# Optimization experiments

Measured on AMD Instinct MI355X. Metric: run time of the kernel, lower is better.

Reference implementation:

```python
import jax, jax.numpy as jnp
import numpy as np

N = 12288
D = 128
NUM_BATCH = 32
EPS = 1e-8


def setup_inputs() -> dict:
    key = jax.random.key(0)
    kq, kk, kv, kb = jax.random.split(key, 4)
    Q = jax.random.normal(kq, (N, D), dtype=jnp.float32)
    K = jax.random.normal(kk, (N, D), dtype=jnp.float32)
    V = jax.random.normal(kv, (N, D), dtype=jnp.float32)
    batch_seg = jnp.sort(jax.random.randint(kb, (N,), 0, NUM_BATCH, dtype=jnp.int32))
    return {"Q": Q, "K": K, "V": V, "num_batch": NUM_BATCH, "batch_seg": batch_seg}


def reference(Q, K, V, num_batch, batch_seg):
    d = Q.shape[-1]
    dot = Q @ K.T                                   # [N, N]
    # NOTE: faithful to original: subtract GLOBAL max, then divide by sqrt(d)
    A = jnp.exp((dot - jnp.max(dot)) / jnp.sqrt(jnp.float32(d)))
    if num_batch > 1:
        mask = (batch_seg[None, :] == batch_seg[:, None])  # block-diagonal
        A = jnp.where(mask, A, jnp.zeros((), A.dtype))
    norm = jnp.sum(A, axis=-1, keepdims=True) + EPS
    A_weights = A / norm
    return A_weights @ V
```

## Files before the change

### kernel.cpp

```cpp
#include <hip/hip_runtime.h>


#define NN 12288
#define DD 128
#define NB 32
#define PS_LD 40
#define VTS 12424

typedef __attribute__((ext_vector_type(8))) short short8;
typedef __attribute__((ext_vector_type(4))) float float4v;

__device__ __forceinline__ short f2bf(float f) {
  unsigned u = __builtin_bit_cast(unsigned, f);
  return (short)((u + 0x7FFFu + ((u >> 16) & 1u)) >> 16);
}

__device__ __forceinline__ short8 ld8_bf16(const float* p) {
  float4v f0 = *(const float4v*)p;
  float4v f1 = *(const float4v*)(p + 4);
  short8 s;
  s[0] = f2bf(f0[0]); s[1] = f2bf(f0[1]); s[2] = f2bf(f0[2]); s[3] = f2bf(f0[3]);
  s[4] = f2bf(f1[0]); s[5] = f2bf(f1[1]); s[6] = f2bf(f1[2]); s[7] = f2bf(f1[3]);
  return s;
}

__device__ __forceinline__ void dma16(const short* gsrc, short* ldst) {
  auto g = (const __attribute__((address_space(1))) void*)(unsigned long long)gsrc;
  auto l = (__attribute__((address_space(3))) void*)(unsigned)(unsigned long long)ldst;
  __builtin_amdgcn_global_load_lds(g, l, 16, 0, 0);
}

__global__ __launch_bounds__(256) void prep_kernel(
    const float* __restrict__ K, const float* __restrict__ V,
    const int* __restrict__ seg,
    short* __restrict__ Kb, short* __restrict__ Vtb, int* __restrict__ starts) {
  const int tid = threadIdx.x;
  const int b = blockIdx.x;
  if (b < 768) {
    const size_t base = (size_t)b * 2048 + (size_t)tid * 8;
    *(short8*)(Kb + base) = ld8_bf16(K + base);
  } else if (b < 864) {
    __shared__ __align__(16) short Ts[DD * 136];
    const int kt = (b - 768) * 128;
#pragma unroll
    for (int rep = 0; rep < 16; ++rep) {
      int v = rep * 256 + tid;
      int key = v >> 5, c4 = (v & 31) * 4;
      float4v f = *(const float4v*)(V + (size_t)(kt + key) * DD + c4);
      Ts[(c4 + 0) * 136 + key] = f2bf(f[0]);
      Ts[(c4 + 1) * 136 + key] = f2bf(f[1]);
      Ts[(c4 + 2) * 136 + key] = f2bf(f[2]);
      Ts[(c4 + 3) * 136 + key] = f2bf(f[3]);
    }
    __syncthreads();
    const int c16 = (tid & 15) * 8;
#pragma unroll
    for (int rep = 0; rep < 8; ++rep) {
      int d = rep * 16 + (tid >> 4);
      short8 s = *(const short8*)&Ts[d * 136 + c16];
      *(short8*)(Vtb + (size_t)d * VTS + kt + c16) = s;
    }
  } else {
    int i = (b - 864) * 256 + tid;
    int s = seg[i];
    int sp = (i == 0) ? -1 : seg[i - 1];
    for (int bb = sp + 1; bb <= s; ++bb) starts[bb] = i;
    if (i == NN - 1)
      for (int bb = s + 1; bb <= NB; ++bb) starts[bb] = NN;
  }
}

__device__ __forceinline__ void issue_tile(
    const short* __restrict__ Kb, const short* __restrict__ Vtb,
    short* KshP, short* VshP, int j0, int wave, int lane) {
#pragma unroll
  for (int i = 0; i < 2; ++i) {
    const int R = wave * 8 + i * 4;
    const int row = R + (lane >> 4);
    const int dchunk = (lane & 15) ^ (row & 15);
    dma16(Kb + (size_t)(j0 + row) * DD + dchunk * 8, KshP + R * 128);
  }
#pragma unroll
  for (int i = 0; i < 2; ++i) {
    const int D = wave * 32 + i * 16;
    const int dr = D + (lane >> 2);
    const int vchunk = (lane & 3) ^ ((lane >> 2) & 3);
    dma16(Vtb + (size_t)dr * VTS + j0 + vchunk * 8, VshP + D * 32);
  }
}

__global__ __launch_bounds__(256, 3) void attn_kernel(
    const float* __restrict__ Q, const short* __restrict__ Kb,
    const short* __restrict__ Vtb, const int* __restrict__ seg,
    const int* __restrict__ starts,
    float* __restrict__ Op, float* __restrict__ lp) {
  __shared__ __align__(16) short Ksh[2][32 * 128];
  __shared__ __align__(16) short Vsh[2][128 * 32];
  __shared__ __align__(16) short Ps[4][16 * PS_LD];

  const int tid = threadIdx.x;
  const int wave = tid >> 6;
  const int lane = tid & 63;
  const int c = lane & 15;
  const int quad = lane >> 4;

  const int bid = blockIdx.x;
  const int y = bid >> 3;
  const int rg = (bid & 7) * 24 + (y >> 2);
  const int sk = y & 3;
  const int i0 = rg * 64;
  const int i0w = i0 + wave * 16;

  const int L = starts[seg[i0]];
  const int H = starts[seg[i0 + 63] + 1];
  const int Lm = L & ~31;
  const int nck = (H - Lm + 31) >> 5;
  const int ck0 = (nck * sk) >> 2;
  const int ck1 = (nck * (sk + 1)) >> 2;
  const int nt = ck1 - ck0;

  int st_r[4], en_r[4];
#pragma unroll
  for (int r = 0; r < 4; ++r) {
    int s = seg[i0w + quad * 4 + r];
    st_r[r] = starts[s];
    en_r[r] = starts[s + 1];
  }

  short8 qf[4];
  {
    const float* qrow = Q + (size_t)(i0w + c) * DD + quad * 8;
#pragma unroll
    for (int kc = 0; kc < 4; ++kc) qf[kc] = ld8_bf16(qrow + kc * 32);
  }

  float4v acc[8];
#pragma unroll
  for (int n = 0; n < 8; ++n) acc[n] = (float4v){0.f, 0.f, 0.f, 0.f};
  float l_part[4] = {0.f, 0.f, 0.f, 0.f};

  const float scale = 0.08838834764831845f;

  if (nt > 0)
    issue_tile(Kb, Vtb, &Ksh[0][0], &Vsh[0][0], Lm + ck0 * 32, wave, lane);
  __syncthreads();

  for (int t = 0; t < nt; ++t) {
    const int j0 = Lm + (ck0 + t) * 32;
    const int p = t & 1;
    if (t + 1 < nt)
      issue_tile(Kb, Vtb, &Ksh[p ^ 1][0], &Vsh[p ^ 1][0], j0 + 32, wave, lane);

    float4v s0 = (float4v){0.f, 0.f, 0.f, 0.f};
    float4v s1 = (float4v){0.f, 0.f, 0.f, 0.f};
    const short* Kp = &Ksh[p][0];
#pragma unroll
    for (int kc = 0; kc < 4; ++kc) {
      const int pos = ((kc * 4 + quad) ^ c) * 8;
      short8 b0 = *(const short8*)(Kp + c * 128 + pos);
      short8 b1 = *(const short8*)(Kp + (16 + c) * 128 + pos);
      s0 = __builtin_amdgcn_mfma_f32_16x16x32_bf16(qf[kc], b0, s0, 0, 0, 0);
      s1 = __builtin_amdgcn_mfma_f32_16x16x32_bf16(qf[kc], b1, s1, 0, 0, 0);
    }

    const int ja = j0 + c, jb = ja + 16;
    short* prow = &Ps[wave][0];
#pragma unroll
    for (int r = 0; r < 4; ++r) {
      float pa = (ja >= st_r[r] && ja < en_r[r]) ? __expf(s0[r] * scale) : 0.f;
      float pb = (jb >= st_r[r] && jb < en_r[r]) ? __expf(s1[r] * scale) : 0.f;
      l_part[r] += pa + pb;
      int row = quad * 4 + r;
      prow[row * PS_LD + c]      = f2bf(pa);
      prow[row * PS_LD + 16 + c] = f2bf(pb);
    }
    short8 pf = *(const short8*)&Ps[wave][c * PS_LD + quad * 8];

    const short* Vp = &Vsh[p][0];
    const int vpos = (quad ^ (c & 3)) * 8;
#pragma unroll
    for (int n = 0; n < 8; ++n) {
      short8 vf = *(const short8*)(Vp + (n * 16 + c) * 32 + vpos);
      acc[n] = __builtin_amdgcn_mfma_f32_16x16x32_bf16(pf, vf, acc[n], 0, 0, 0);
    }

    __syncthreads();
  }

  float lrow[4];
#pragma unroll
  for (int r = 0; r < 4; ++r) {
    float l = l_part[r];
    l += __shfl_xor(l, 1, 64);
    l += __shfl_xor(l, 2, 64);
    l += __shfl_xor(l, 4, 64);
    l += __shfl_xor(l, 8, 64);
    lrow[r] = l;
  }

  float* OpW = Op + ((size_t)sk * NN + i0w) * DD;
#pragma unroll
  for (int n = 0; n < 8; ++n)
#pragma unroll
    for (int r = 0; r < 4; ++r)
      OpW[(quad * 4 + r) * DD + n * 16 + c] = acc[n][r];
  if (c == 0) {
#pragma unroll
    for (int r = 0; r < 4; ++r) lp[sk * NN + i0w + quad * 4 + r] = lrow[r];
  }
}

__global__ __launch_bounds__(256) void combine_kernel(
    const float* __restrict__ Op, const float* __restrict__ lp,
    float* __restrict__ out) {
  const int idx = blockIdx.x * 256 + threadIdx.x;
#pragma unroll
  for (int rep = 0; rep < 2; ++rep) {
    int u = idx + rep * 196608;
    int row = u >> 5, c4 = (u & 31) * 4;
    float l = lp[row] + lp[NN + row] + lp[2 * NN + row] + lp[3 * NN + row];
    float4v o = (float4v){0.f, 0.f, 0.f, 0.f};
#pragma unroll
    for (int s = 0; s < 4; ++s) {
      float4v t = *(const float4v*)(Op + ((size_t)s * NN + row) * DD + c4);
      o[0] += t[0]; o[1] += t[1]; o[2] += t[2]; o[3] += t[3];
    }
    float inv = 1.f / (l + 1e-8f);
    o[0] *= inv; o[1] *= inv; o[2] *= inv; o[3] *= inv;
    *(float4v*)(out + (size_t)row * DD + c4) = o;
  }
}

#define KT_LD 136
#define VT_LD 40
typedef __attribute__((ext_vector_type(4))) short short4v;

__global__ __launch_bounds__(256) void attn_fallback(
    const float* __restrict__ Q, const float* __restrict__ K,
    const float* __restrict__ V, const int* __restrict__ seg,
    float* __restrict__ out) {
  __shared__ __align__(16) short Kt[32 * KT_LD];
  __shared__ __align__(16) short Vt[DD * VT_LD];
  __shared__ __align__(16) short Ps[4][16 * PS_LD];
  const int tid = threadIdx.x, wave = tid >> 6, lane = tid & 63;
  const int c = lane & 15, quad = lane >> 4;
  const int m0 = blockIdx.x * 64, i0 = m0 + wave * 16;
  const int segFirst = seg[m0], segLast = seg[m0 + 63];
  int lo = 0, hb = NN;
  while (lo < hb) { int mid = (lo + hb) >> 1; if (seg[mid] < segFirst) lo = mid + 1; else hb = mid; }
  int hi = lo, hb2 = NN;
  while (hi < hb2) { int mid = (hi + hb2) >> 1; if (seg[mid] <= segLast) hi = mid + 1; else hb2 = mid; }
  short8 qf[4];
  const float* qrow = Q + (size_t)(i0 + c) * DD + quad * 8;
#pragma unroll
  for (int kc = 0; kc < 4; ++kc) qf[kc] = ld8_bf16(qrow + kc * 32);
  int seg_r[4];
#pragma unroll
  for (int r = 0; r < 4; ++r) seg_r[r] = seg[i0 + quad * 4 + r];
  float4v acc[8];
#pragma unroll
  for (int n = 0; n < 8; ++n) acc[n] = (float4v){0.f, 0.f, 0.f, 0.f};
  float l_part[4] = {0.f, 0.f, 0.f, 0.f};
  const float scale = 0.08838834764831845f;
  for (int j0 = lo; j0 < hi; j0 += 32) {
    __syncthreads();
    {
      int row = tid >> 3, ch = tid & 7;
      int jj = j0 + row; if (jj > NN - 1) jj = NN - 1;
      const float* kp = K + (size_t)jj * DD + ch * 16;
      short* dst = &Kt[row * KT_LD + ch * 16];
#pragma unroll
      for (int q4 = 0; q4 < 4; ++q4) {
        float4v f = *(const float4v*)(kp + q4 * 4);
        short4v s;
        s[0] = f2bf(f[0]); s[1] = f2bf(f[1]); s[2] = f2bf(f[2]); s[3] = f2bf(f[3]);
        *(short4v*)(dst + q4 * 4) = s;
      }
    }
    {
      int d = tid & 127, jh = tid >> 7;
      float vv[16];
#pragma unroll
      for (int j = 0; j < 16; ++j) {
        int jj = j0 + jh * 16 + j; if (jj > NN - 1) jj = NN - 1;
        vv[j] = V[(size_t)jj * DD + d];
      }
      short8 a, b2;
#pragma unroll
      for (int j = 0; j < 8; ++j) { a[j] = f2bf(vv[j]); b2[j] = f2bf(vv[8 + j]); }
      *(short8*)&Vt[d * VT_LD + jh * 16] = a;
      *(short8*)&Vt[d * VT_LD + jh * 16 + 8] = b2;
    }
    __syncthreads();
    float4v s0 = (float4v){0.f, 0.f, 0.f, 0.f};
    float4v s1 = (float4v){0.f, 0.f, 0.f, 0.f};
    const short* krow0 = &Kt[c * KT_LD + quad * 8];
    const short* krow1 = &Kt[(16 + c) * KT_LD + quad * 8];
#pragma unroll
    for (int kc = 0; kc < 4; ++kc) {
      short8 b0 = *(const short8*)(krow0 + kc * 32);
      short8 b1 = *(const short8*)(krow1 + kc * 32);
      s0 = __builtin_amdgcn_mfma_f32_16x16x32_bf16(qf[kc], b0, s0, 0, 0, 0);
      s1 = __builtin_amdgcn_mfma_f32_16x16x32_bf16(qf[kc], b1, s1, 0, 0, 0);
    }
    int ja = j0 + c, jb = ja + 16;
    int sa = seg[ja < NN ? ja : NN - 1];
    int sb = seg[jb < NN ? jb : NN - 1];
    bool va = ja < hi, vb = jb < hi;
    short* prow = &Ps[wave][0];
#pragma unroll
    for (int r = 0; r < 4; ++r) {
      float pa = (va && sa == seg_r[r]) ? __expf(s0[r] * scale) : 0.f;
      float pb = (vb && sb == seg_r[r]) ? __expf(s1[r] * scale) : 0.f;
      l_part[r] += pa + pb;
      int row = quad * 4 + r;
      prow[row * PS_LD + c] = f2bf(pa);
      prow[row * PS_LD + 16 + c] = f2bf(pb);
    }
    short8 pf = *(const short8*)&Ps[wave][c * PS_LD + quad * 8];
#pragma unroll
    for (int n = 0; n < 8; ++n) {
      short8 vfr = *(const short8*)&Vt[(n * 16 + c) * VT_LD + quad * 8];
      acc[n] = __builtin_amdgcn_mfma_f32_16x16x32_bf16(pf, vfr, acc[n], 0, 0, 0);
    }
  }
  float linv[4];
#pragma unroll
  for (int r = 0; r < 4; ++r) {
    float l = l_part[r];
    l += __shfl_xor(l, 1, 64);
    l += __shfl_xor(l, 2, 64);
    l += __shfl_xor(l, 4, 64);
    l += __shfl_xor(l, 8, 64);
    linv[r] = 1.f / (l + 1e-8f);
  }
#pragma unroll
  for (int n = 0; n < 8; ++n)
#pragma unroll
    for (int r = 0; r < 4; ++r)
      out[(size_t)(i0 + quad * 4 + r) * DD + n * 16 + c] = acc[n][r] * linv[r];
}

extern "C" void kernel_launch(void* const* d_in, const int* in_sizes, int n_in,
                              void* d_out, int out_size, void* d_ws, size_t ws_size,
                              hipStream_t stream) {
  const float* Q = (const float*)d_in[0];
  const float* K = (const float*)d_in[1];
  const float* V = (const float*)d_in[2];
  const int* seg = (const int*)d_in[4];
  float* out = (float*)d_out;

  const size_t kb_bytes = (size_t)NN * DD * sizeof(short);
  const size_t vt_bytes = (size_t)DD * VTS * sizeof(short);
  const size_t st_bytes = 64 * sizeof(int);
  const size_t op_bytes = (size_t)4 * NN * DD * sizeof(float);
  const size_t lp_bytes = (size_t)4 * NN * sizeof(float);
  const size_t need = kb_bytes + vt_bytes + st_bytes + op_bytes + lp_bytes;

  if (ws_size >= need) {
    char* w = (char*)d_ws;
    short* Kb  = (short*)w;                     w += kb_bytes;
    short* Vtb = (short*)w;                     w += vt_bytes;
    int* starts = (int*)w;                      w += st_bytes;
    float* Op = (float*)w;                      w += op_bytes;
    float* lp = (float*)w;
    prep_kernel<<<864 + NN / 256, 256, 0, stream>>>(K, V, seg, Kb, Vtb, starts);
    attn_kernel<<<768, 256, 0, stream>>>(Q, Kb, Vtb, seg, starts, Op, lp);
    combine_kernel<<<768, 256, 0, stream>>>(Op, lp, out);
  } else {
    attn_fallback<<<NN / 64, 256, 0, stream>>>(Q, K, V, seg, out);
  }
}
```

Before: 96.40 us.

## Fuse split-K combine into attention kernel via last-arriver atomic counter

Removes the separate combine kernel launch. Each row group's four split-K blocks increment a per-row-group counter after a threadfence, and whichever block arrives last reduces the four partial outputs and normalizers and writes the final output. The counters are zeroed by an extra block in the prep kernel. This saves a kernel launch and its tail, at the cost of atomics, fences, and a serialized combine tail on the last block of each group.

```diff
diff --git a/kernel.cpp b/kernel.cpp
--- a/kernel.cpp
+++ b/kernel.cpp
@@ -33,7 +33,8 @@
 __global__ __launch_bounds__(256) void prep_kernel(
     const float* __restrict__ K, const float* __restrict__ V,
     const int* __restrict__ seg,
-    short* __restrict__ Kb, short* __restrict__ Vtb, int* __restrict__ starts) {
+    short* __restrict__ Kb, short* __restrict__ Vtb, int* __restrict__ starts,
+    unsigned* __restrict__ cnt) {
   const int tid = threadIdx.x;
   const int b = blockIdx.x;
   if (b < 768) {
@@ -60,13 +61,15 @@
       short8 s = *(const short8*)&Ts[d * 136 + c16];
       *(short8*)(Vtb + (size_t)d * VTS + kt + c16) = s;
     }
-  } else {
+  } else if (b < 912) {
     int i = (b - 864) * 256 + tid;
     int s = seg[i];
     int sp = (i == 0) ? -1 : seg[i - 1];
     for (int bb = sp + 1; bb <= s; ++bb) starts[bb] = i;
     if (i == NN - 1)
       for (int bb = s + 1; bb <= NB; ++bb) starts[bb] = NN;
+  } else {
+    if (tid < 192) cnt[tid] = 0u;
   }
 }
 
@@ -93,10 +96,12 @@
     const float* __restrict__ Q, const short* __restrict__ Kb,
     const short* __restrict__ Vtb, const int* __restrict__ seg,
     const int* __restrict__ starts,
-    float* __restrict__ Op, float* __restrict__ lp) {
+    float* __restrict__ Op, float* __restrict__ lp,
+    unsigned* __restrict__ cnt, float* __restrict__ out) {
   __shared__ __align__(16) short Ksh[2][32 * 128];
   __shared__ __align__(16) short Vsh[2][128 * 32];
   __shared__ __align__(16) short Ps[4][16 * PS_LD];
+  __shared__ int sflag;
 
   const int tid = threadIdx.x;
   const int wave = tid >> 6;
@@ -208,26 +213,29 @@
 #pragma unroll
     for (int r = 0; r < 4; ++r) lp[sk * NN + i0w + quad * 4 + r] = lrow[r];
   }
-}
-
-__global__ __launch_bounds__(256) void combine_kernel(
-    const float* __restrict__ Op, const float* __restrict__ lp,
-    float* __restrict__ out) {
-  const int idx = blockIdx.x * 256 + threadIdx.x;
-#pragma unroll
-  for (int rep = 0; rep < 2; ++rep) {
-    int u = idx + rep * 196608;
-    int row = u >> 5, c4 = (u & 31) * 4;
-    float l = lp[row] + lp[NN + row] + lp[2 * NN + row] + lp[3 * NN + row];
-    float4v o = (float4v){0.f, 0.f, 0.f, 0.f};
-#pragma unroll
-    for (int s = 0; s < 4; ++s) {
-      float4v t = *(const float4v*)(Op + ((size_t)s * NN + row) * DD + c4);
-      o[0] += t[0]; o[1] += t[1]; o[2] += t[2]; o[3] += t[3];
-    }
-    float inv = 1.f / (l + 1e-8f);
-    o[0] *= inv; o[1] *= inv; o[2] *= inv; o[3] *= inv;
-    *(float4v*)(out + (size_t)row * DD + c4) = o;
+
+  __threadfence();
+  __syncthreads();
+  if (tid == 0) sflag = (atomicAdd(&cnt[rg], 1u) == 3u);
+  __syncthreads();
+  if (sflag) {
+    __threadfence();
+#pragma unroll
+    for (int rep = 0; rep < 8; ++rep) {
+      int u = rep * 256 + tid;
+      int row = u >> 5, c4 = (u & 31) * 4;
+      int grow = i0 + row;
+      float l = lp[grow] + lp[NN + grow] + lp[2 * NN + grow] + lp[3 * NN + grow];
+      float4v o = (float4v){0.f, 0.f, 0.f, 0.f};
+#pragma unroll
+      for (int s = 0; s < 4; ++s) {
+        float4v t = *(const float4v*)(Op + ((size_t)s * NN + grow) * DD + c4);
+        o[0] += t[0]; o[1] += t[1]; o[2] += t[2]; o[3] += t[3];
+      }
+      float inv = 1.f / (l + 1e-8f);
+      o[0] *= inv; o[1] *= inv; o[2] *= inv; o[3] *= inv;
+      *(float4v*)(out + (size_t)grow * DD + c4) = o;
+    }
   }
 }
 
@@ -355,7 +363,8 @@
   const size_t st_bytes = 64 * sizeof(int);
   const size_t op_bytes = (size_t)4 * NN * DD * sizeof(float);
   const size_t lp_bytes = (size_t)4 * NN * sizeof(float);
-  const size_t need = kb_bytes + vt_bytes + st_bytes + op_bytes + lp_bytes;
+  const size_t ct_bytes = 192 * sizeof(unsigned);
+  const size_t need = kb_bytes + vt_bytes + st_bytes + op_bytes + lp_bytes + ct_bytes;
 
   if (ws_size >= need) {
     char* w = (char*)d_ws;
@@ -363,10 +372,10 @@
     short* Vtb = (short*)w;                     w += vt_bytes;
     int* starts = (int*)w;                      w += st_bytes;
     float* Op = (float*)w;                      w += op_bytes;
-    float* lp = (float*)w;
-    prep_kernel<<<864 + NN / 256, 256, 0, stream>>>(K, V, seg, Kb, Vtb, starts);
-    attn_kernel<<<768, 256, 0, stream>>>(Q, Kb, Vtb, seg, starts, Op, lp);
-    combine_kernel<<<768, 256, 0, stream>>>(Op, lp, out);
+    float* lp = (float*)w;                      w += lp_bytes;
+    unsigned* cnt = (unsigned*)w;
+    prep_kernel<<<913, 256, 0, stream>>>(K, V, seg, Kb, Vtb, starts, cnt);
+    attn_kernel<<<768, 256, 0, stream>>>(Q, Kb, Vtb, seg, starts, Op, lp, cnt, out);
   } else {
     attn_fallback<<<NN / 64, 256, 0, stream>>>(Q, K, V, seg, out);
   }
```

After: 221.7 us. 2.3x slower.
